# Performance work log

Hardware: AMD Instinct MI355X
Metric: run time of the kernel (lower is better)

Reference implementation:

```python
import jax, jax.numpy as jnp
import numpy as np

N = 8192       # number of graph nodes
F_IN = 33      # 2*trajectory_length + 1
HID = 32       # n_hidden in GAT layers
MLP_H = 128    # num_hiddens_action
A_OUT = 27     # num_outputs_action
NEG_INF = -1e9


def setup_inputs() -> dict:
    key = jax.random.key(0)
    ks = jax.random.split(key, 12)
    def p(k, shape, scale=0.1):
        return jax.random.normal(k, shape, dtype=jnp.float32) * scale
    return {
        "x": jax.random.normal(ks[0], (N, F_IN), dtype=jnp.float32),
        "adj": jax.random.uniform(ks[1], (N, N, 1), dtype=jnp.float32),
        "W1": p(ks[2], (F_IN, HID)),  "a1": p(ks[3], (2 * HID,)),
        "W2": p(ks[4], (HID, HID)),   "a2": p(ks[5], (2 * HID,)),
        "W3": p(ks[6], (HID, F_IN)),  "a3": p(ks[7], (2 * F_IN,)),
        "Wm1": p(ks[8], (F_IN, MLP_H)), "bm1": jnp.zeros((MLP_H,), jnp.float32),
        "Wm2": p(ks[9], (MLP_H, A_OUT)), "bm2": jnp.zeros((A_OUT,), jnp.float32),
    }


def _gat(x, mask, W, a):
    # Single-head GAT layer (labml-style): score_ij = LeakyReLU(a . [g_i || g_j])
    g = x @ W                                  # [N, d]
    d = g.shape[-1]
    s_src = g @ a[:d]                          # [N]
    s_dst = g @ a[d:]                          # [N]
    e = jax.nn.leaky_relu(s_src[:, None] + s_dst[None, :], 0.2)  # [N, N]
    e = jnp.where(mask, e, NEG_INF)
    att = jax.nn.softmax(e, axis=1)            # softmax over neighbors j
    return att @ g                             # [N, d]


def reference(x, adj, W1, a1, W2, a2, W3, a3, Wm1, bm1, Wm2, bm2):
    mask = adj[..., 0] > 0.5                   # [N, N] boolean adjacency
    h = jax.nn.elu(_gat(x, mask, W1, a1))      # layer1 + ELU (dropout = eval identity)
    h = jax.nn.elu(_gat(h, mask, W2, a2))      # layer2 + ELU
    h = _gat(h, mask, W3, a3)                  # output layer (is_concat=False, 1 head)
    hid = jax.nn.leaky_relu(h[0] @ Wm1 + bm1, 0.01)  # mlp_forward on node 0
    return hid @ Wm2 + bm2
```

## Files before the change

### kernel.cpp

```cpp
#include <hip/hip_runtime.h>
#include <cstdint>
#include <cstddef>

namespace {
constexpr int NN     = 8192;
constexpr int DD     = 32;
constexpr int ROWS   = 128;
constexpr int TJ     = 64;
constexpr int JSPLIT = 16;
constexpr int JRANGE = NN / JSPLIT;
constexpr int WORDS  = NN / 64;
constexpr int STR    = 72;
}

typedef __attribute__((ext_vector_type(8))) short short8;
typedef __attribute__((ext_vector_type(4))) float floatx4;

__device__ __forceinline__ unsigned short f2bf(float f) {
  unsigned int u = __float_as_uint(f);
  u += 0x7fffu + ((u >> 16) & 1u);
  return (unsigned short)(u >> 16);
}

template<int DIN, int DOUT, bool FROMACC>
__global__ void k_g(const float* __restrict__ in,
                    const float* __restrict__ den,
                    const float* __restrict__ W,
                    const float* __restrict__ avec,
                    float* __restrict__ g,
                    unsigned short* __restrict__ gT,
                    float* __restrict__ ssrc,
                    float* __restrict__ sdst)
{
  __shared__ float Ws[DIN * DOUT];
  __shared__ float as[2 * DOUT];
  const int t = threadIdx.x;
  for (int idx = t; idx < DIN * DOUT; idx += 128) Ws[idx] = W[idx];
  if (t < 2 * DOUT) as[t] = avec[t];
  __syncthreads();

  const int i = blockIdx.x * 128 + t;
  float h[DIN];
  if (FROMACC) {
    const float dinv = 1.0f / den[i];
    #pragma unroll
    for (int k = 0; k < DIN; k++) {
      const float v = in[(size_t)i * DIN + k] * dinv;
      h[k] = v > 0.f ? v : (__expf(v) - 1.0f);
    }
  } else {
    #pragma unroll
    for (int k = 0; k < DIN; k++) h[k] = in[(size_t)i * DIN + k];
  }
  float ss = 0.f, sd = 0.f;
  #pragma unroll 4
  for (int d = 0; d < DOUT; d++) {
    float a = 0.f;
    #pragma unroll
    for (int k = 0; k < DIN; k++) a += h[k] * Ws[k * DOUT + d];
    if (g)  g[(size_t)i * DOUT + d] = a;
    if (gT) gT[(size_t)d * NN + i] = f2bf(a);
    ss += a * as[d];
    sd += a * as[DOUT + d];
  }
  ssrc[i] = ss;
  sdst[i] = sd;
}

template<int LAYER>
__global__ __launch_bounds__(256, 4)
void k_att(const float* __restrict__ adj,
           unsigned long long* __restrict__ mask64,
           const unsigned short* __restrict__ gT,
           const float* __restrict__ ssrc,
           const float* __restrict__ sdst,
           float* __restrict__ hacc,
           float* __restrict__ den)
{
  __shared__ unsigned short wt[ROWS * STR];
  __shared__ unsigned short gt[DD * STR];

  const int t    = threadIdx.x;
  const int lane = t & 63;
  const int wv   = __builtin_amdgcn_readfirstlane(t >> 6);
  const int quad = lane >> 4;
  const int m16  = lane & 15;
  const int rb   = (blockIdx.x / JSPLIT) * ROWS;
  const int j0   = (blockIdx.x % JSPLIT) * JRANGE;
  const int r0   = wv * 32;

  floatx4 acc[2][2];
  floatx4 dacc[2];
  #pragma unroll
  for (int a = 0; a < 2; a++) {
    dacc[a] = (floatx4){0.f, 0.f, 0.f, 0.f};
    #pragma unroll
    for (int b = 0; b < 2; b++) acc[a][b] = (floatx4){0.f, 0.f, 0.f, 0.f};
  }
  short8 ones;
  #pragma unroll
  for (int k = 0; k < 8; k++) ones[k] = (short)0x3F80;

  const int sdrow = t >> 3;
  const int soff  = (t & 7) * 8;

  for (int jt = j0; jt < j0 + JRANGE; jt += TJ) {
    const short8 gvld = *reinterpret_cast<const short8*>(&gT[(size_t)sdrow * NN + jt + soff]);
    const float sdj = sdst[jt + lane];

    if constexpr (LAYER == 1) {
      float av[32];
      #pragma unroll
      for (int ii = 0; ii < 32; ii++)
        av[ii] = adj[(size_t)(rb + r0 + ii) * NN + jt + lane];
      #pragma unroll
      for (int ii = 0; ii < 32; ii++) {
        const int iu = rb + r0 + ii;
        const float sa = ssrc[iu];
        const bool m = av[ii] > 0.5f;
        const unsigned long long bal = __ballot(m);
        if (lane == 0) mask64[(size_t)iu * WORDS + (jt >> 6)] = bal;
        const float e = sa + sdj;
        const float w = m ? __expf(fmaxf(e, 0.2f * e)) : 0.f;
        wt[(r0 + ii) * STR + lane] = f2bf(w);
      }
    } else {
      #pragma unroll
      for (int ii = 0; ii < 32; ii++) {
        const int iu = rb + r0 + ii;
        const float sa = ssrc[iu];
        const unsigned long long mw = mask64[(size_t)iu * WORDS + (jt >> 6)];
        const bool m = (mw >> lane) & 1ull;
        const float e = sa + sdj;
        const float w = m ? __expf(fmaxf(e, 0.2f * e)) : 0.f;
        wt[(r0 + ii) * STR + lane] = f2bf(w);
      }
    }
    *reinterpret_cast<short8*>(&gt[sdrow * STR + soff]) = gvld;
    __syncthreads();

    #pragma unroll
    for (int ks = 0; ks < 2; ks++) {
      const int ko = ks * 32 + quad * 8;
      const short8 bf0 = *reinterpret_cast<const short8*>(&gt[m16 * STR + ko]);
      const short8 bf1 = *reinterpret_cast<const short8*>(&gt[(16 + m16) * STR + ko]);
      #pragma unroll
      for (int mt = 0; mt < 2; mt++) {
        const short8 af = *reinterpret_cast<const short8*>(&wt[(r0 + mt * 16 + m16) * STR + ko]);
        acc[mt][0] = __builtin_amdgcn_mfma_f32_16x16x32_bf16(af, bf0, acc[mt][0], 0, 0, 0);
        acc[mt][1] = __builtin_amdgcn_mfma_f32_16x16x32_bf16(af, bf1, acc[mt][1], 0, 0, 0);
        dacc[mt]   = __builtin_amdgcn_mfma_f32_16x16x32_bf16(af, ones, dacc[mt], 0, 0, 0);
      }
    }
    __syncthreads();
  }

  #pragma unroll
  for (int mt = 0; mt < 2; mt++) {
    const int rr = rb + r0 + mt * 16 + quad * 4;
    #pragma unroll
    for (int r = 0; r < 4; r++) {
      atomicAdd(&hacc[(size_t)(rr + r) * DD + m16],      acc[mt][0][r]);
      atomicAdd(&hacc[(size_t)(rr + r) * DD + 16 + m16], acc[mt][1][r]);
    }
    if (m16 == 0) {
      #pragma unroll
      for (int r = 0; r < 4; r++) atomicAdd(&den[rr + r], dacc[mt][r]);
    }
  }
}

__global__ void k_att3(const unsigned long long* __restrict__ mask64,
                       const float* __restrict__ g3,
                       const float* __restrict__ ssrc,
                       const float* __restrict__ sdst,
                       float* __restrict__ o3,
                       float* __restrict__ den3)
{
  __shared__ float wl[256];
  const int t = threadIdx.x;
  const int jb = blockIdx.x * 256;
  const int j = jb + t;
  const unsigned long long mw = mask64[j >> 6];
  const bool m = (mw >> (j & 63)) & 1ull;
  const float e = ssrc[0] + sdst[j];
  const float w = m ? __expf(fmaxf(e, 0.2f * e)) : 0.f;
  wl[t] = w;
  float v = w;
  #pragma unroll
  for (int s = 32; s > 0; s >>= 1) v += __shfl_xor(v, s, 64);
  if ((t & 63) == 0) atomicAdd(den3, v);
  __syncthreads();
  for (int idx = t; idx < 33 * 8; idx += 256) {
    const int d = idx % 33;
    const int oct = idx / 33;
    float s = 0.f;
    for (int jj = 0; jj < 32; jj++)
      s += wl[oct * 32 + jj] * g3[(size_t)(jb + oct * 32 + jj) * 33 + d];
    atomicAdd(&o3[d], s);
  }
}

__global__ void k_mlp(const float* __restrict__ o3, const float* __restrict__ den3,
                      const float* __restrict__ Wm1, const float* __restrict__ bm1,
                      const float* __restrict__ Wm2, const float* __restrict__ bm2,
                      float* __restrict__ out)
{
  __shared__ float h0[33];
  __shared__ float hid[128];
  const int t = threadIdx.x;
  if (t < 33) h0[t] = o3[t] / den3[0];
  __syncthreads();
  float a = bm1[t];
  for (int k = 0; k < 33; k++) a += h0[k] * Wm1[k * 128 + t];
  hid[t] = fmaxf(a, 0.01f * a);
  __syncthreads();
  if (t < 27) {
    float o = bm2[t];
    for (int k = 0; k < 128; k++) o += hid[k] * Wm2[k * 27 + t];
    out[t] = o;
  }
}

extern "C" void kernel_launch(void* const* d_in, const int* in_sizes, int n_in,
                              void* d_out, int out_size, void* d_ws, size_t ws_size,
                              hipStream_t stream)
{
  const float* x   = (const float*)d_in[0];
  const float* adj = (const float*)d_in[1];
  const float* W1  = (const float*)d_in[2];
  const float* a1  = (const float*)d_in[3];
  const float* W2  = (const float*)d_in[4];
  const float* a2  = (const float*)d_in[5];
  const float* W3  = (const float*)d_in[6];
  const float* a3  = (const float*)d_in[7];
  const float* Wm1 = (const float*)d_in[8];
  const float* bm1 = (const float*)d_in[9];
  const float* Wm2 = (const float*)d_in[10];
  const float* bm2 = (const float*)d_in[11];
  float* out = (float*)d_out;
  (void)in_sizes; (void)n_in; (void)out_size; (void)ws_size;

  char* ws = (char*)d_ws;
  size_t off = 0;
  auto alloc = [&](size_t bytes) -> void* {
    void* p = ws + off;
    off = (off + bytes + 255) & ~(size_t)255;
    return p;
  };
  float* g3  = (float*)alloc((size_t)NN * 33 * 4);
  float* s1s = (float*)alloc((size_t)NN * 4);
  float* s1d = (float*)alloc((size_t)NN * 4);
  float* s2s = (float*)alloc((size_t)NN * 4);
  float* s2d = (float*)alloc((size_t)NN * 4);
  float* s3s = (float*)alloc((size_t)NN * 4);
  float* s3d = (float*)alloc((size_t)NN * 4);
  char* zbase = ws + off;
  float* h1acc = (float*)alloc((size_t)NN * DD * 4);
  float* den1  = (float*)alloc((size_t)NN * 4);
  float* h2acc = (float*)alloc((size_t)NN * DD * 4);
  float* den2  = (float*)alloc((size_t)NN * 4);
  float* o3    = (float*)alloc(64 * 4);
  float* den3  = (float*)alloc(64 * 4);
  const size_t zbytes = (size_t)((ws + off) - zbase);
  unsigned long long* mask64 = (unsigned long long*)alloc((size_t)NN * WORDS * 8);
  unsigned short* g1T = (unsigned short*)alloc((size_t)DD * NN * 2);
  unsigned short* g2T = (unsigned short*)alloc((size_t)DD * NN * 2);

  hipMemsetAsync(zbase, 0, zbytes, stream);
  k_g<33, 32, false><<<NN / 128, 128, 0, stream>>>(x, nullptr, W1, a1, nullptr, g1T, s1s, s1d);
  k_att<1><<<(NN / ROWS) * JSPLIT, 256, 0, stream>>>(adj, mask64, g1T, s1s, s1d, h1acc, den1);
  k_g<32, 32, true><<<NN / 128, 128, 0, stream>>>(h1acc, den1, W2, a2, nullptr, g2T, s2s, s2d);
  k_att<2><<<(NN / ROWS) * JSPLIT, 256, 0, stream>>>(nullptr, mask64, g2T, s2s, s2d, h2acc, den2);
  k_g<32, 33, true><<<NN / 128, 128, 0, stream>>>(h2acc, den2, W3, a3, g3, nullptr, s3s, s3d);
  k_att3<<<NN / 256, 256, 0, stream>>>(mask64, g3, s3s, s3d, o3, den3);
  k_mlp<<<1, 128, 0, stream>>>(o3, den3, Wm1, bm1, Wm2, bm2, out);
}
```

Before: 535.1 us.

## Use per-wave LDS tiles, double j-tile, read g directly from global, widen k_g

The attention kernel now gives each wave its own LDS weight tile and loads the g^T B-fragments directly from global memory, which removes both block-wide __syncthreads per tile. The j-tile doubles to 128 so each lane handles two columns with float2 adj loads and packed bf16 stores. Because lane l now owns columns 2l and 2l+1, the mask bits are stored interleaved, and k_att3 indexing is changed to match. The feature-projection kernel for layers 1 and 2 is rewritten to use 4 threads per row with a transposed weight layout in LDS. Skipping the LDS staging means redundant global or L2 traffic for the gT fragments across waves.

New measurement: 489.1 us. -8.6%, faster.

```diff
diff --git a/kernel.cpp b/kernel.cpp
--- a/kernel.cpp
+++ b/kernel.cpp
@@ -6,11 +6,11 @@
 constexpr int NN     = 8192;
 constexpr int DD     = 32;
 constexpr int ROWS   = 128;
-constexpr int TJ     = 64;
+constexpr int TJ     = 128;
 constexpr int JSPLIT = 16;
 constexpr int JRANGE = NN / JSPLIT;
 constexpr int WORDS  = NN / 64;
-constexpr int STR    = 72;
+constexpr int STR2   = 136;
 }
 
 typedef __attribute__((ext_vector_type(8))) short short8;
@@ -22,13 +22,69 @@
   return (unsigned short)(u >> 16);
 }
 
-template<int DIN, int DOUT, bool FROMACC>
+template<int DIN, bool FROMACC>
+__global__ void k_g32(const float* __restrict__ in,
+                      const float* __restrict__ den,
+                      const float* __restrict__ W,
+                      const float* __restrict__ avec,
+                      unsigned short* __restrict__ gT,
+                      float* __restrict__ ssrc,
+                      float* __restrict__ sdst)
+{
+  __shared__ float WsT[32 * 36];
+  __shared__ float as[64];
+  const int t = threadIdx.x;
+  for (int idx = t; idx < DIN * 32; idx += 256) {
+    const int k = idx / 32, d = idx % 32;
+    WsT[d * 36 + k] = W[idx];
+  }
+  if (t < 64) as[t] = avec[t];
+  __syncthreads();
+
+  const int r  = t >> 2;
+  const int dg = t & 3;
+  const int i  = blockIdx.x * 64 + r;
+
+  float h[DIN];
+  if (FROMACC) {
+    const float dinv = 1.0f / den[i];
+    #pragma unroll
+    for (int k = 0; k < DIN; k++) {
+      const float v = in[(size_t)i * DIN + k] * dinv;
+      h[k] = v > 0.f ? v : (__expf(v) - 1.0f);
+    }
+  } else {
+    #pragma unroll
+    for (int k = 0; k < DIN; k++) h[k] = in[(size_t)i * DIN + k];
+  }
+
+  float ss = 0.f, sd = 0.f;
+  #pragma unroll
+  for (int d8 = 0; d8 < 8; d8++) {
+    const int d = dg * 8 + d8;
+    float a = 0.f;
+    #pragma unroll
+    for (int kb = 0; kb < DIN / 4; kb++) {
+      const float4 wv = *reinterpret_cast<const float4*>(&WsT[d * 36 + kb * 4]);
+      a += h[kb * 4] * wv.x + h[kb * 4 + 1] * wv.y + h[kb * 4 + 2] * wv.z + h[kb * 4 + 3] * wv.w;
+    }
+    #pragma unroll
+    for (int k = (DIN / 4) * 4; k < DIN; k++) a += h[k] * WsT[d * 36 + k];
+    gT[(size_t)d * NN + i] = f2bf(a);
+    ss += a * as[d];
+    sd += a * as[32 + d];
+  }
+  ss += __shfl_xor(ss, 1, 64); ss += __shfl_xor(ss, 2, 64);
+  sd += __shfl_xor(sd, 1, 64); sd += __shfl_xor(sd, 2, 64);
+  if (dg == 0) { ssrc[i] = ss; sdst[i] = sd; }
+}
+
+template<int DIN, int DOUT>
 __global__ void k_g(const float* __restrict__ in,
                     const float* __restrict__ den,
                     const float* __restrict__ W,
                     const float* __restrict__ avec,
                     float* __restrict__ g,
-                    unsigned short* __restrict__ gT,
                     float* __restrict__ ssrc,
                     float* __restrict__ sdst)
 {
@@ -41,16 +97,11 @@
 
   const int i = blockIdx.x * 128 + t;
   float h[DIN];
-  if (FROMACC) {
-    const float dinv = 1.0f / den[i];
-    #pragma unroll
-    for (int k = 0; k < DIN; k++) {
-      const float v = in[(size_t)i * DIN + k] * dinv;
-      h[k] = v > 0.f ? v : (__expf(v) - 1.0f);
-    }
-  } else {
-    #pragma unroll
-    for (int k = 0; k < DIN; k++) h[k] = in[(size_t)i * DIN + k];
+  const float dinv = 1.0f / den[i];
+  #pragma unroll
+  for (int k = 0; k < DIN; k++) {
+    const float v = in[(size_t)i * DIN + k] * dinv;
+    h[k] = v > 0.f ? v : (__expf(v) - 1.0f);
   }
   float ss = 0.f, sd = 0.f;
   #pragma unroll 4
@@ -58,8 +109,7 @@
     float a = 0.f;
     #pragma unroll
     for (int k = 0; k < DIN; k++) a += h[k] * Ws[k * DOUT + d];
-    if (g)  g[(size_t)i * DOUT + d] = a;
-    if (gT) gT[(size_t)d * NN + i] = f2bf(a);
+    g[(size_t)i * DOUT + d] = a;
     ss += a * as[d];
     sd += a * as[DOUT + d];
   }
@@ -77,8 +127,7 @@
            float* __restrict__ hacc,
            float* __restrict__ den)
 {
-  __shared__ unsigned short wt[ROWS * STR];
-  __shared__ unsigned short gt[DD * STR];
+  __shared__ unsigned short wt[4][32 * STR2];
 
   const int t    = threadIdx.x;
   const int lane = t & 63;
@@ -88,6 +137,7 @@
   const int rb   = (blockIdx.x / JSPLIT) * ROWS;
   const int j0   = (blockIdx.x % JSPLIT) * JRANGE;
   const int r0   = wv * 32;
+  unsigned short* wtw = wt[wv];
 
   floatx4 acc[2][2];
   floatx4 dacc[2];
@@ -101,58 +151,68 @@
   #pragma unroll
   for (int k = 0; k < 8; k++) ones[k] = (short)0x3F80;
 
-  const int sdrow = t >> 3;
-  const int soff  = (t & 7) * 8;
-
   for (int jt = j0; jt < j0 + JRANGE; jt += TJ) {
-    const short8 gvld = *reinterpret_cast<const short8*>(&gT[(size_t)sdrow * NN + jt + soff]);
-    const float sdj = sdst[jt + lane];
-
-    if constexpr (LAYER == 1) {
-      float av[32];
-      #pragma unroll
-      for (int ii = 0; ii < 32; ii++)
-        av[ii] = adj[(size_t)(rb + r0 + ii) * NN + jt + lane];
-      #pragma unroll
-      for (int ii = 0; ii < 32; ii++) {
-        const int iu = rb + r0 + ii;
-        const float sa = ssrc[iu];
-        const bool m = av[ii] > 0.5f;
-        const unsigned long long bal = __ballot(m);
-        if (lane == 0) mask64[(size_t)iu * WORDS + (jt >> 6)] = bal;
-        const float e = sa + sdj;
-        const float w = m ? __expf(fmaxf(e, 0.2f * e)) : 0.f;
-        wt[(r0 + ii) * STR + lane] = f2bf(w);
+    const float2 sd01 = *reinterpret_cast<const float2*>(&sdst[jt + 2 * lane]);
+
+    #pragma unroll
+    for (int hb = 0; hb < 2; hb++) {
+      if constexpr (LAYER == 1) {
+        float2 av[16];
+        #pragma unroll
+        for (int ii = 0; ii < 16; ii++)
+          av[ii] = *reinterpret_cast<const float2*>(
+              &adj[(size_t)(rb + r0 + hb * 16 + ii) * NN + jt + 2 * lane]);
+        #pragma unroll
+        for (int ii = 0; ii < 16; ii++) {
+          const int il = hb * 16 + ii;
+          const int iu = rb + r0 + il;
+          const float sa = ssrc[iu];
+          const bool m0 = av[ii].x > 0.5f;
+          const bool m1 = av[ii].y > 0.5f;
+          const unsigned long long b0 = __ballot(m0);
+          const unsigned long long b1 = __ballot(m1);
+          if (lane == 0) {
+            ulonglong2 bb; bb.x = b0; bb.y = b1;
+            *reinterpret_cast<ulonglong2*>(&mask64[(size_t)iu * WORDS + (jt >> 6)]) = bb;
+          }
+          const float e0 = sa + sd01.x, e1 = sa + sd01.y;
+          const float w0 = m0 ? __expf(fmaxf(e0, 0.2f * e0)) : 0.f;
+          const float w1 = m1 ? __expf(fmaxf(e1, 0.2f * e1)) : 0.f;
+          const unsigned int pk = (unsigned int)f2bf(w0) | ((unsigned int)f2bf(w1) << 16);
+          *reinterpret_cast<unsigned int*>(&wtw[il * STR2 + 2 * lane]) = pk;
+        }
+      } else {
+        #pragma unroll
+        for (int ii = 0; ii < 16; ii++) {
+          const int il = hb * 16 + ii;
+          const int iu = rb + r0 + il;
+          const float sa = ssrc[iu];
+          const ulonglong2 mw = *reinterpret_cast<const ulonglong2*>(
+              &mask64[(size_t)iu * WORDS + (jt >> 6)]);
+          const bool m0 = (mw.x >> lane) & 1ull;
+          const bool m1 = (mw.y >> lane) & 1ull;
+          const float e0 = sa + sd01.x, e1 = sa + sd01.y;
+          const float w0 = m0 ? __expf(fmaxf(e0, 0.2f * e0)) : 0.f;
+          const float w1 = m1 ? __expf(fmaxf(e1, 0.2f * e1)) : 0.f;
+          const unsigned int pk = (unsigned int)f2bf(w0) | ((unsigned int)f2bf(w1) << 16);
+          *reinterpret_cast<unsigned int*>(&wtw[il * STR2 + 2 * lane]) = pk;
+        }
       }
-    } else {
-      #pragma unroll
-      for (int ii = 0; ii < 32; ii++) {
-        const int iu = rb + r0 + ii;
-        const float sa = ssrc[iu];
-        const unsigned long long mw = mask64[(size_t)iu * WORDS + (jt >> 6)];
-        const bool m = (mw >> lane) & 1ull;
-        const float e = sa + sdj;
-        const float w = m ? __expf(fmaxf(e, 0.2f * e)) : 0.f;
-        wt[(r0 + ii) * STR + lane] = f2bf(w);
-      }
-    }
-    *reinterpret_cast<short8*>(&gt[sdrow * STR + soff]) = gvld;
-    __syncthreads();
-
-    #pragma unroll
-    for (int ks = 0; ks < 2; ks++) {
+    }
+
+    #pragma unroll
+    for (int ks = 0; ks < 4; ks++) {
       const int ko = ks * 32 + quad * 8;
-      const short8 bf0 = *reinterpret_cast<const short8*>(&gt[m16 * STR + ko]);
-      const short8 bf1 = *reinterpret_cast<const short8*>(&gt[(16 + m16) * STR + ko]);
+      const short8 bf0 = *reinterpret_cast<const short8*>(&gT[(size_t)m16 * NN + jt + ko]);
+      const short8 bf1 = *reinterpret_cast<const short8*>(&gT[(size_t)(16 + m16) * NN + jt + ko]);
       #pragma unroll
       for (int mt = 0; mt < 2; mt++) {
-        const short8 af = *reinterpret_cast<const short8*>(&wt[(r0 + mt * 16 + m16) * STR + ko]);
+        const short8 af = *reinterpret_cast<const short8*>(&wtw[(mt * 16 + m16) * STR2 + ko]);
         acc[mt][0] = __builtin_amdgcn_mfma_f32_16x16x32_bf16(af, bf0, acc[mt][0], 0, 0, 0);
         acc[mt][1] = __builtin_amdgcn_mfma_f32_16x16x32_bf16(af, bf1, acc[mt][1], 0, 0, 0);
         dacc[mt]   = __builtin_amdgcn_mfma_f32_16x16x32_bf16(af, ones, dacc[mt], 0, 0, 0);
       }
     }
-    __syncthreads();
   }
 
   #pragma unroll
@@ -181,8 +241,8 @@
   const int t = threadIdx.x;
   const int jb = blockIdx.x * 256;
   const int j = jb + t;
-  const unsigned long long mw = mask64[j >> 6];
-  const bool m = (mw >> (j & 63)) & 1ull;
+  const unsigned long long mw = mask64[((j >> 7) << 1) | (j & 1)];
+  const bool m = (mw >> ((j >> 1) & 63)) & 1ull;
   const float e = ssrc[0] + sdst[j];
   const float w = m ? __expf(fmaxf(e, 0.2f * e)) : 0.f;
   wl[t] = w;
@@ -268,11 +328,11 @@
   unsigned short* g2T = (unsigned short*)alloc((size_t)DD * NN * 2);
 
   hipMemsetAsync(zbase, 0, zbytes, stream);
-  k_g<33, 32, false><<<NN / 128, 128, 0, stream>>>(x, nullptr, W1, a1, nullptr, g1T, s1s, s1d);
+  k_g32<33, false><<<NN / 64, 256, 0, stream>>>(x, nullptr, W1, a1, g1T, s1s, s1d);
   k_att<1><<<(NN / ROWS) * JSPLIT, 256, 0, stream>>>(adj, mask64, g1T, s1s, s1d, h1acc, den1);
-  k_g<32, 32, true><<<NN / 128, 128, 0, stream>>>(h1acc, den1, W2, a2, nullptr, g2T, s2s, s2d);
+  k_g32<32, true><<<NN / 64, 256, 0, stream>>>(h1acc, den1, W2, a2, g2T, s2s, s2d);
   k_att<2><<<(NN / ROWS) * JSPLIT, 256, 0, stream>>>(nullptr, mask64, g2T, s2s, s2d, h2acc, den2);
-  k_g<32, 33, true><<<NN / 128, 128, 0, stream>>>(h2acc, den2, W3, a3, g3, nullptr, s3s, s3d);
+  k_g<32, 33><<<NN / 128, 128, 0, stream>>>(h2acc, den2, W3, a3, g3, s3s, s3d);
   k_att3<<<NN / 256, 256, 0, stream>>>(mask64, g3, s3s, s3d, o3, den3);
   k_mlp<<<1, 128, 0, stream>>>(o3, den3, Wm1, bm1, Wm2, bm2, out);
 }
```
